# Kernel tuning notes

Hardware: AMD Instinct MI355X
Metric: run time of the kernel (lower is better)

Reference implementation:

```python
import jax, jax.numpy as jnp
import numpy as np

N_NODES = 50000
N_EDGES = 1600000


def setup_inputs() -> dict:
    key = jax.random.key(0)
    ks = jax.random.split(key, 8)
    dims = [1024, 2048, 1024, 512]
    fea = jax.random.normal(ks[0], (N_NODES, dims[0]), dtype=jnp.float32)
    edge_index = jax.random.randint(ks[1], (2, N_EDGES), 0, N_NODES, dtype=jnp.int64)
    edge_vals = jax.random.uniform(ks[2], (N_EDGES,), dtype=jnp.float32)
    # Glorot-ish scaled weights per GCN layer
    W1 = jax.random.normal(ks[3], (dims[0], dims[1]), dtype=jnp.float32) / np.sqrt(dims[0])
    W2 = jax.random.normal(ks[4], (dims[1], dims[2]), dtype=jnp.float32) / np.sqrt(dims[1])
    W3 = jax.random.normal(ks[5], (dims[2], dims[3]), dtype=jnp.float32) / np.sqrt(dims[2])
    b1 = jnp.zeros((dims[1],), dtype=jnp.float32)
    b2 = jnp.zeros((dims[2],), dtype=jnp.float32)
    b3 = jnp.zeros((dims[3],), dtype=jnp.float32)
    return {"fea": fea, "edge_index": edge_index, "edge_vals": edge_vals,
            "W1": W1, "b1": b1, "W2": W2, "b2": b2, "W3": W3, "b3": b3}


def _gcn_layer(x, row, col, edge_vals, W, b):
    # dense transform: [N, din] @ [din, dout] + bias
    support = x @ W + b
    # spmm(adj, support) in COO form: out[row] += val * support[col]
    msgs = support[col] * edge_vals[:, None]          # [E, dout]
    return jax.ops.segment_sum(msgs, row, num_segments=N_NODES)


def reference(fea, edge_index, edge_vals, W1, b1, W2, b2, W3, b3):
    row, col = edge_index[0], edge_index[1]
    h = jax.nn.relu(_gcn_layer(fea, row, col, edge_vals, W1, b1))
    h = jax.nn.relu(_gcn_layer(h, row, col, edge_vals, W2, b2))
    # last layer: no activation
    return _gcn_layer(h, row, col, edge_vals, W3, b3)
```

## Files before the change

### kernel.cpp

```cpp
#include <hip/hip_runtime.h>

typedef unsigned short u16;
using bf16x8 = __attribute__((ext_vector_type(8))) short;
using u16x8  = __attribute__((ext_vector_type(8))) unsigned short;
using f32x4  = __attribute__((ext_vector_type(4))) float;

#define NN 50000
#define NPAD 50176

__device__ __forceinline__ u16 f2b(float f) {
  union { float f; unsigned u; } x; x.f = f;
  unsigned r = x.u + 0x7fffu + ((x.u >> 16) & 1u);
  return (u16)(r >> 16);
}
__device__ __forceinline__ float b2f(u16 h) {
  union { unsigned u; float f; } x; x.u = ((unsigned)h) << 16; return x.f;
}

#define GLOAD_LDS16(g, l) __builtin_amdgcn_global_load_lds( \
    (const __attribute__((address_space(1))) unsigned int*)(g), \
    (__attribute__((address_space(3))) unsigned int*)(l), 16, 0, 0)

__global__ void hist_kernel(const int* __restrict__ rows, const float* __restrict__ vals,
                            int* __restrict__ counts, float* __restrict__ rowsum, int E) {
  int e = blockIdx.x * 256 + threadIdx.x;
  if (e < E) {
    int r = rows[e];
    atomicAdd(&counts[r], 1);
    atomicAdd(&rowsum[r], vals[e]);
  }
}

__global__ void scan_bsum(const int* __restrict__ counts, int* __restrict__ bsum, int n) {
  __shared__ int s[256];
  int t = threadIdx.x;
  int gi = blockIdx.x * 256 + t;
  s[t] = (gi < n) ? counts[gi] : 0;
  __syncthreads();
  for (int d = 128; d > 0; d >>= 1) {
    if (t < d) s[t] += s[t + d];
    __syncthreads();
  }
  if (t == 0) bsum[blockIdx.x] = s[0];
}

__global__ void scan_partials(int* __restrict__ bsum, int nb) {
  __shared__ int s[256];
  int t = threadIdx.x;
  int v = (t < nb) ? bsum[t] : 0;
  s[t] = v;
  __syncthreads();
  for (int d = 1; d < 256; d <<= 1) {
    int x = (t >= d) ? s[t - d] : 0;
    __syncthreads();
    s[t] += x;
    __syncthreads();
  }
  if (t < nb) bsum[t] = s[t] - v;
}

__global__ void scan_final(const int* __restrict__ counts, const int* __restrict__ bsum,
                           int* __restrict__ offs, int n) {
  __shared__ int s[256];
  int t = threadIdx.x;
  int gi = blockIdx.x * 256 + t;
  int v = (gi < n) ? counts[gi] : 0;
  s[t] = v;
  __syncthreads();
  for (int d = 1; d < 256; d <<= 1) {
    int x = (t >= d) ? s[t - d] : 0;
    __syncthreads();
    s[t] += x;
    __syncthreads();
  }
  if (gi <= n) offs[gi] = bsum[blockIdx.x] + s[t] - v;
}

__global__ void scatter_kernel(const int* __restrict__ rows, const int* __restrict__ cols,
                               const float* __restrict__ vals, const int* __restrict__ offs,
                               int* __restrict__ cursor, int* __restrict__ ecol,
                               float* __restrict__ ev2, int E) {
  int e = blockIdx.x * 256 + threadIdx.x;
  if (e < E) {
    int r = rows[e];
    int p = offs[r] + atomicAdd(&cursor[r], 1);
    ecol[p] = cols[e];
    ev2[p] = vals[e];
  }
}

__global__ void conv_f2b4(const float* __restrict__ in, u16* __restrict__ out, int n4) {
  int i = blockIdx.x * 256 + threadIdx.x;
  if (i < n4) {
    float4 f = ((const float4*)in)[i];
    ushort4 o;
    o.x = f2b(f.x); o.y = f2b(f.y); o.z = f2b(f.z); o.w = f2b(f.w);
    ((ushort4*)out)[i] = o;
  }
}

__global__ void transpose_conv(const float* __restrict__ W, u16* __restrict__ Wt, int K, int N) {
  __shared__ float tile[32][33];
  int bx = blockIdx.x * 32;
  int by = blockIdx.y * 32;
  int tx = threadIdx.x;
  int ty = threadIdx.y;
  for (int i = 0; i < 32; i += 8) tile[ty + i][tx] = W[(size_t)(by + ty + i) * N + bx + tx];
  __syncthreads();
  for (int i = 0; i < 32; i += 8) Wt[(size_t)(bx + ty + i) * K + by + tx] = f2b(tile[tx][ty + i]);
}

__global__ __launch_bounds__(512, 2)
void gemm256(const u16* __restrict__ A, const u16* __restrict__ Bt,
             const float* __restrict__ bias, const float* __restrict__ rowsum,
             u16* __restrict__ C, int M, int N, int K, int relu, int nbx) {
  __shared__ __align__(16) u16 As[2][256 * 64];
  __shared__ __align__(16) u16 Bs[2][256 * 64];

  const int p = blockIdx.x, total = gridDim.x;
  const int q = total >> 3, r8 = total & 7;
  const int xcd = p & 7, slot_ = p >> 3;
  const int l = (xcd < r8 ? xcd * (q + 1) : r8 * (q + 1) + (xcd - r8) * q) + slot_;
  const int bm = (l / nbx) * 256;
  const int bn = (l % nbx) * 256;

  const int tid = threadIdx.x;
  const int lane = tid & 63;
  const int wid = tid >> 6;
  const int wm = wid >> 2;
  const int wn = wid & 3;
  const int l15 = lane & 15, lg = lane >> 4;

  const int xcol = (tid & 7) ^ ((tid >> 3) & 7);
  const u16* gA = A + (size_t)(bm + (tid >> 3)) * K + xcol * 8;
  const u16* gB = Bt + (size_t)(bn + (tid >> 3)) * K + xcol * 8;
  const size_t rowstep = (size_t)64 * K;

  f32x4 acc[8][4];
#pragma unroll
  for (int i = 0; i < 8; i++)
#pragma unroll
    for (int j = 0; j < 4; j++)
#pragma unroll
      for (int k = 0; k < 4; k++) acc[i][j][k] = 0.f;

  const int NT = K >> 6;

#define STAGE(kt, b)                                                           \
  {                                                                            \
    const u16* sa = gA + (size_t)(kt) * 64;                                    \
    const u16* sb = gB + (size_t)(kt) * 64;                                    \
    u16* da = &As[b][0] + tid * 8;                                             \
    u16* db = &Bs[b][0] + tid * 8;                                             \
    GLOAD_LDS16(sa, da);                                                       \
    GLOAD_LDS16(sa + rowstep, da + 4096);                                      \
    GLOAD_LDS16(sa + 2 * rowstep, da + 8192);                                  \
    GLOAD_LDS16(sa + 3 * rowstep, da + 12288);                                 \
    GLOAD_LDS16(sb, db);                                                       \
    GLOAD_LDS16(sb + rowstep, db + 4096);                                      \
    GLOAD_LDS16(sb + 2 * rowstep, db + 8192);                                  \
    GLOAD_LDS16(sb + 3 * rowstep, db + 12288);                                 \
  }

  STAGE(0, 0);

  for (int u = 0; u < NT; u++) {
    const int cb = u & 1;
    if (u + 1 < NT) {
      STAGE(u + 1, cb ^ 1);
      asm volatile("s_waitcnt vmcnt(8)" ::: "memory");
    } else {
      asm volatile("s_waitcnt vmcnt(0)" ::: "memory");
    }
    __builtin_amdgcn_s_barrier();

    const u16* ab = &As[cb][0];
    const u16* bb = &Bs[cb][0];

    bf16x8 bf[4][2];
#pragma unroll
    for (int n = 0; n < 4; n++)
#pragma unroll
      for (int s = 0; s < 2; s++) {
        int row = wn * 64 + n * 16 + l15;
        int slot = (s * 4 + lg) ^ (row & 7);
        bf[n][s] = *(const bf16x8*)&bb[row * 64 + slot * 8];
      }
    bf16x8 af0[4][2];
#pragma unroll
    for (int m = 0; m < 4; m++)
#pragma unroll
      for (int s = 0; s < 2; s++) {
        int row = wm * 128 + m * 16 + l15;
        int slot = (s * 4 + lg) ^ (row & 7);
        af0[m][s] = *(const bf16x8*)&ab[row * 64 + slot * 8];
      }
    __builtin_amdgcn_s_setprio(1);
#pragma unroll
    for (int m = 0; m < 4; m++)
#pragma unroll
      for (int n = 0; n < 4; n++) {
        acc[m][n] = __builtin_amdgcn_mfma_f32_16x16x32_bf16(af0[m][0], bf[n][0], acc[m][n], 0, 0, 0);
        acc[m][n] = __builtin_amdgcn_mfma_f32_16x16x32_bf16(af0[m][1], bf[n][1], acc[m][n], 0, 0, 0);
      }
    __builtin_amdgcn_s_setprio(0);
    bf16x8 af1[4][2];
#pragma unroll
    for (int m = 0; m < 4; m++)
#pragma unroll
      for (int s = 0; s < 2; s++) {
        int row = wm * 128 + (m + 4) * 16 + l15;
        int slot = (s * 4 + lg) ^ (row & 7);
        af1[m][s] = *(const bf16x8*)&ab[row * 64 + slot * 8];
      }
    asm volatile("s_waitcnt lgkmcnt(0)" ::: "memory");
    __builtin_amdgcn_s_barrier();
    __builtin_amdgcn_s_setprio(1);
#pragma unroll
    for (int m = 0; m < 4; m++)
#pragma unroll
      for (int n = 0; n < 4; n++) {
        acc[m + 4][n] = __builtin_amdgcn_mfma_f32_16x16x32_bf16(af1[m][0], bf[n][0], acc[m + 4][n], 0, 0, 0);
        acc[m + 4][n] = __builtin_amdgcn_mfma_f32_16x16x32_bf16(af1[m][1], bf[n][1], acc[m + 4][n], 0, 0, 0);
      }
    __builtin_amdgcn_s_setprio(0);
  }
#undef STAGE

  float bs[4];
#pragma unroll
  for (int n = 0; n < 4; n++) bs[n] = bias[bn + wn * 64 + n * 16 + l15];
#pragma unroll
  for (int m = 0; m < 8; m++) {
    int rowb = bm + wm * 128 + m * 16 + lg * 4;
#pragma unroll
    for (int j = 0; j < 4; j++) {
      int row = rowb + j;
      if (row < M) {
        float rs = rowsum ? rowsum[row] : 1.0f;
#pragma unroll
        for (int n = 0; n < 4; n++) {
          int col = bn + wn * 64 + n * 16 + l15;
          float v = acc[m][n][j] + rs * bs[n];
          if (relu) v = fmaxf(v, 0.f);
          C[(size_t)row * N + col] = f2b(v);
        }
      }
    }
  }
}

template <int VEC, int RELU, int OUTF32>
__global__ __launch_bounds__(64)
void spmm3(const int* __restrict__ offs, const int* __restrict__ ecol,
           const float* __restrict__ ev, const u16* __restrict__ X,
           void* __restrict__ outp, int stride) {
  const int node = blockIdx.x;
  const int t = threadIdx.x;
  const int s0 = offs[node];
  const int e0 = offs[node + 1];
  float acc[VEC];
#pragma unroll
  for (int k = 0; k < VEC; k++) acc[k] = 0.f;
  const u16* __restrict__ Xc = X + (size_t)t * VEC;

  int j = s0;
  for (; j + 4 <= e0; j += 4) {
    const int c0 = ecol[j], c1 = ecol[j + 1], c2 = ecol[j + 2], c3 = ecol[j + 3];
    const float v0 = ev[j], v1 = ev[j + 1], v2 = ev[j + 2], v3 = ev[j + 3];
    u16 a0[VEC], a1[VEC], a2[VEC], a3[VEC];
    if constexpr (VEC == 8) {
      *(u16x8*)a0 = *(const u16x8*)(Xc + (size_t)c0 * stride);
      *(u16x8*)a1 = *(const u16x8*)(Xc + (size_t)c1 * stride);
      *(u16x8*)a2 = *(const u16x8*)(Xc + (size_t)c2 * stride);
      *(u16x8*)a3 = *(const u16x8*)(Xc + (size_t)c3 * stride);
    } else {
      *(ushort4*)a0 = *(const ushort4*)(Xc + (size_t)c0 * stride);
      *(ushort4*)a1 = *(const ushort4*)(Xc + (size_t)c1 * stride);
      *(ushort4*)a2 = *(const ushort4*)(Xc + (size_t)c2 * stride);
      *(ushort4*)a3 = *(const ushort4*)(Xc + (size_t)c3 * stride);
    }
#pragma unroll
    for (int k = 0; k < VEC; k++) acc[k] += v0 * b2f(a0[k]);
#pragma unroll
    for (int k = 0; k < VEC; k++) acc[k] += v1 * b2f(a1[k]);
#pragma unroll
    for (int k = 0; k < VEC; k++) acc[k] += v2 * b2f(a2[k]);
#pragma unroll
    for (int k = 0; k < VEC; k++) acc[k] += v3 * b2f(a3[k]);
  }
  for (; j < e0; j++) {
    const int c0 = ecol[j];
    const float v0 = ev[j];
    u16 a0[VEC];
    if constexpr (VEC == 8) {
      *(u16x8*)a0 = *(const u16x8*)(Xc + (size_t)c0 * stride);
    } else {
      *(ushort4*)a0 = *(const ushort4*)(Xc + (size_t)c0 * stride);
    }
#pragma unroll
    for (int k = 0; k < VEC; k++) acc[k] += v0 * b2f(a0[k]);
  }

  if (RELU) {
#pragma unroll
    for (int k = 0; k < VEC; k++) acc[k] = fmaxf(acc[k], 0.f);
  }
  if (OUTF32) {
    float* o = (float*)outp + (size_t)node * stride + (size_t)t * VEC;
#pragma unroll
    for (int k = 0; k < VEC; k += 4) {
      float4 st;
      st.x = acc[k]; st.y = acc[k + 1]; st.z = acc[k + 2]; st.w = acc[k + 3];
      *(float4*)(o + k) = st;
    }
  } else {
    u16* o = (u16*)outp + (size_t)node * stride + (size_t)t * VEC;
    if constexpr (VEC == 8) {
      u16x8 st;
#pragma unroll
      for (int k = 0; k < 8; k++) st[k] = f2b(acc[k]);
      *(u16x8*)o = st;
    } else {
      ushort4 st;
      st.x = f2b(acc[0]); st.y = f2b(acc[1]); st.z = f2b(acc[2]); st.w = f2b(acc[3]);
      *(ushort4*)o = st;
    }
  }
}

extern "C" void kernel_launch(void* const* d_in, const int* in_sizes, int n_in,
                              void* d_out, int out_size, void* d_ws, size_t ws_size,
                              hipStream_t stream) {
  const float* fea = (const float*)d_in[0];
  const int* ei = (const int*)d_in[1];
  const float* ev = (const float*)d_in[2];
  const float* W1 = (const float*)d_in[3];
  const float* b1 = (const float*)d_in[4];
  const float* W2 = (const float*)d_in[5];
  const float* b2 = (const float*)d_in[6];
  const float* W3 = (const float*)d_in[7];
  const float* b3 = (const float*)d_in[8];
  const int E = in_sizes[1] / 2;
  const int* erow = ei;
  const int* ecol_in = ei + E;

  char* w = (char*)d_ws;
  auto alloc = [&](size_t bytes) {
    char* p = w;
    w += (bytes + 255) & ~(size_t)255;
    return p;
  };
  u16* fea_b = (u16*)alloc((size_t)NPAD * 1024 * 2);
  u16* bufB  = (u16*)alloc((size_t)NPAD * 1024 * 2);
  u16* h1_b  = (u16*)alloc((size_t)NPAD * 2048 * 2);
  u16* t2_b  = (u16*)alloc((size_t)NPAD * 1024 * 2);
  u16* W1t = (u16*)alloc((size_t)2048 * 1024 * 2);
  u16* W2t = (u16*)alloc((size_t)1024 * 2048 * 2);
  u16* W3t = (u16*)alloc((size_t)512 * 1024 * 2);
  float* rowsum = (float*)alloc((size_t)NN * 4);
  int* counts = (int*)alloc((size_t)NN * 4);
  int* cursor = (int*)alloc((size_t)NN * 4);
  int* offs = (int*)alloc((size_t)(NN + 1) * 4);
  int* ecol = (int*)alloc((size_t)E * 4);
  float* ev2 = (float*)alloc((size_t)E * 4);
  int* bsum = (int*)alloc(256 * 4);
  (void)bsum; (void)ws_size; (void)n_in; (void)out_size;

  hipMemsetAsync(rowsum, 0, (size_t)((char*)offs - (char*)rowsum), stream);

  const int eb = (E + 255) / 256;
  const int nb = (NN + 256) / 256;
  hist_kernel<<<eb, 256, 0, stream>>>(erow, ev, counts, rowsum, E);
  scan_bsum<<<nb, 256, 0, stream>>>(counts, bsum, NN);
  scan_partials<<<1, 256, 0, stream>>>(bsum, nb);
  scan_final<<<nb, 256, 0, stream>>>(counts, bsum, offs, NN);
  scatter_kernel<<<eb, 256, 0, stream>>>(erow, ecol_in, ev, offs, cursor, ecol, ev2, E);

  conv_f2b4<<<(NN * 1024 / 4 + 255) / 256, 256, 0, stream>>>(fea, fea_b, NN * 1024 / 4);
  dim3 tb(32, 8);
  transpose_conv<<<dim3(2048 / 32, 1024 / 32), tb, 0, stream>>>(W1, W1t, 1024, 2048);
  transpose_conv<<<dim3(1024 / 32, 2048 / 32), tb, 0, stream>>>(W2, W2t, 2048, 1024);
  transpose_conv<<<dim3(512 / 32, 1024 / 32), tb, 0, stream>>>(W3, W3t, 1024, 512);

  const int MT2 = (NN + 255) / 256;
  spmm3<8, 0, 0><<<NN, 64, 0, stream>>>(offs, ecol, ev2, fea_b, bufB, 1024);
  spmm3<8, 0, 0><<<NN, 64, 0, stream>>>(offs, ecol, ev2, fea_b + 512, bufB + 512, 1024);
  gemm256<<<(2048 / 256) * MT2, 512, 0, stream>>>(bufB, W1t, b1, rowsum, h1_b, NN, 2048, 1024, 1, 2048 / 256);
  gemm256<<<(1024 / 256) * MT2, 512, 0, stream>>>(h1_b, W2t, b2, nullptr, t2_b, NN, 1024, 2048, 0, 1024 / 256);
  spmm3<8, 1, 0><<<NN, 64, 0, stream>>>(offs, ecol, ev2, t2_b, fea_b, 1024);
  spmm3<8, 1, 0><<<NN, 64, 0, stream>>>(offs, ecol, ev2, t2_b + 512, fea_b + 512, 1024);
  gemm256<<<(512 / 256) * MT2, 512, 0, stream>>>(fea_b, W3t, b3, nullptr, bufB, NN, 512, 1024, 0, 512 / 256);
  spmm3<4, 0, 1><<<NN, 64, 0, stream>>>(offs, ecol, ev2, bufB, d_out, 512);
  spmm3<4, 0, 1><<<NN, 64, 0, stream>>>(offs, ecol, ev2, bufB + 256, (float*)d_out + 256, 512);
}
```

Measured before the change: 2.103 ms.

## Slice features into 32-column node-contiguous panels for cache-friendly SpMM gathers

The input features and the GEMM outputs that feed SpMM are now stored in a sliced layout: 32-column panels, each holding all nodes contiguously. The SpMM kernel is rewritten so each wave handles one node and one 32-column pass, with four edge groups of 16 lanes reduced by shuffles. Each pass's gather footprint is 64 bytes per node, so the working set per pass fits in L2/MALL and random-row reuse improves. The cost is 64-byte gathers instead of 1 KB row segments per node, extra reduction shuffles, and scattered 2-byte GEMM epilogue stores.

```diff
diff --git a/kernel.cpp b/kernel.cpp
--- a/kernel.cpp
+++ b/kernel.cpp
@@ -89,14 +89,20 @@
   }
 }
 
-__global__ void conv_f2b4(const float* __restrict__ in, u16* __restrict__ out, int n4) {
-  int i = blockIdx.x * 256 + threadIdx.x;
-  if (i < n4) {
-    float4 f = ((const float4*)in)[i];
-    ushort4 o;
-    o.x = f2b(f.x); o.y = f2b(f.y); o.z = f2b(f.z); o.w = f2b(f.w);
-    ((ushort4*)out)[i] = o;
-  }
+__global__ void repack_fea(const float* __restrict__ fea, u16* __restrict__ Xs) {
+  int g = blockIdx.x * 256 + threadIdx.x;
+  if (g >= NN * 128) return;
+  int node = g >> 7;
+  int k = g & 127;
+  const float* src = fea + (size_t)node * 1024 + k * 8;
+  float4 f0 = *(const float4*)src;
+  float4 f1 = *(const float4*)(src + 4);
+  u16x8 o;
+  o[0] = f2b(f0.x); o[1] = f2b(f0.y); o[2] = f2b(f0.z); o[3] = f2b(f0.w);
+  o[4] = f2b(f1.x); o[5] = f2b(f1.y); o[6] = f2b(f1.z); o[7] = f2b(f1.w);
+  int pass = k >> 2;
+  int off = (k & 3) * 8;
+  *(u16x8*)(Xs + (size_t)pass * (NN * 32) + (size_t)node * 32 + off) = o;
 }
 
 __global__ void transpose_conv(const float* __restrict__ W, u16* __restrict__ Wt, int K, int N) {
@@ -113,7 +119,7 @@
 __global__ __launch_bounds__(512, 2)
 void gemm256(const u16* __restrict__ A, const u16* __restrict__ Bt,
              const float* __restrict__ bias, const float* __restrict__ rowsum,
-             u16* __restrict__ C, int M, int N, int K, int relu, int nbx) {
+             u16* __restrict__ C, int M, int N, int K, int relu, int nbx, int sliced) {
   __shared__ __align__(16) u16 As[2][256 * 64];
   __shared__ __align__(16) u16 Bs[2][256 * 64];
 
@@ -243,88 +249,75 @@
           int col = bn + wn * 64 + n * 16 + l15;
           float v = acc[m][n][j] + rs * bs[n];
           if (relu) v = fmaxf(v, 0.f);
-          C[(size_t)row * N + col] = f2b(v);
+          if (!sliced) {
+            C[(size_t)row * N + col] = f2b(v);
+          } else {
+            C[(size_t)(col >> 5) * ((size_t)NN * 32) + (size_t)row * 32 + (col & 31)] = f2b(v);
+          }
         }
       }
     }
   }
 }
 
-template <int VEC, int RELU, int OUTF32>
-__global__ __launch_bounds__(64)
-void spmm3(const int* __restrict__ offs, const int* __restrict__ ecol,
-           const float* __restrict__ ev, const u16* __restrict__ X,
+template <int RELU, int OUTF32>
+__global__ __launch_bounds__(1024)
+void spmm4(const int* __restrict__ offs, const int* __restrict__ ecol,
+           const float* __restrict__ ev, const u16* __restrict__ Xs,
            void* __restrict__ outp, int stride) {
-  const int node = blockIdx.x;
-  const int t = threadIdx.x;
-  const int s0 = offs[node];
-  const int e0 = offs[node + 1];
-  float acc[VEC];
-#pragma unroll
-  for (int k = 0; k < VEC; k++) acc[k] = 0.f;
-  const u16* __restrict__ Xc = X + (size_t)t * VEC;
-
+  const int wid = threadIdx.x >> 6;
+  const int lane = threadIdx.x & 63;
+  const int e2 = lane >> 4;
+  const int c16 = lane & 15;
+  const int bpp = NN / 16;
+  const int pass = blockIdx.x / bpp;
+  const int b = blockIdx.x % bpp;
+  const int q = bpp >> 3, r = bpp & 7;
+  const int xcd = b & 7, slot = b >> 3;
+  const int lb = (xcd < r ? xcd * (q + 1) : r * (q + 1) + (xcd - r) * q) + slot;
+  const int node = lb * 16 + wid;
+
+  const u16* __restrict__ Xp = Xs + (size_t)pass * (NN * 32) + c16 * 2;
+  const int s0 = offs[node], e0 = offs[node + 1];
+  float a0 = 0.f, a1 = 0.f;
   int j = s0;
-  for (; j + 4 <= e0; j += 4) {
-    const int c0 = ecol[j], c1 = ecol[j + 1], c2 = ecol[j + 2], c3 = ecol[j + 3];
-    const float v0 = ev[j], v1 = ev[j + 1], v2 = ev[j + 2], v3 = ev[j + 3];
-    u16 a0[VEC], a1[VEC], a2[VEC], a3[VEC];
-    if constexpr (VEC == 8) {
-      *(u16x8*)a0 = *(const u16x8*)(Xc + (size_t)c0 * stride);
-      *(u16x8*)a1 = *(const u16x8*)(Xc + (size_t)c1 * stride);
-      *(u16x8*)a2 = *(const u16x8*)(Xc + (size_t)c2 * stride);
-      *(u16x8*)a3 = *(const u16x8*)(Xc + (size_t)c3 * stride);
+  for (; j + 8 <= e0; j += 8) {
+    int ca = ecol[j + e2], cb = ecol[j + 4 + e2];
+    float va = ev[j + e2], vb = ev[j + 4 + e2];
+    unsigned pa = *(const unsigned*)(Xp + (size_t)ca * 32);
+    unsigned pb = *(const unsigned*)(Xp + (size_t)cb * 32);
+    a0 += va * b2f((u16)pa);
+    a1 += va * b2f((u16)(pa >> 16));
+    a0 += vb * b2f((u16)pb);
+    a1 += vb * b2f((u16)(pb >> 16));
+  }
+  if (j + 4 <= e0) {
+    int ca = ecol[j + e2];
+    float va = ev[j + e2];
+    unsigned pa = *(const unsigned*)(Xp + (size_t)ca * 32);
+    a0 += va * b2f((u16)pa);
+    a1 += va * b2f((u16)(pa >> 16));
+    j += 4;
+  }
+  if (e2 < e0 - j) {
+    int ca = ecol[j + e2];
+    float va = ev[j + e2];
+    unsigned pa = *(const unsigned*)(Xp + (size_t)ca * 32);
+    a0 += va * b2f((u16)pa);
+    a1 += va * b2f((u16)(pa >> 16));
+  }
+  a0 += __shfl_xor(a0, 16);
+  a1 += __shfl_xor(a1, 16);
+  a0 += __shfl_xor(a0, 32);
+  a1 += __shfl_xor(a1, 32);
+  if (RELU) { a0 = fmaxf(a0, 0.f); a1 = fmaxf(a1, 0.f); }
+  if (e2 == 0) {
+    if (OUTF32) {
+      float2 st; st.x = a0; st.y = a1;
+      *(float2*)((float*)outp + (size_t)node * stride + pass * 32 + c16 * 2) = st;
     } else {
-      *(ushort4*)a0 = *(const ushort4*)(Xc + (size_t)c0 * stride);
-      *(ushort4*)a1 = *(const ushort4*)(Xc + (size_t)c1 * stride);
-      *(ushort4*)a2 = *(const ushort4*)(Xc + (size_t)c2 * stride);
-      *(ushort4*)a3 = *(const ushort4*)(Xc + (size_t)c3 * stride);
-    }
-#pragma unroll
-    for (int k = 0; k < VEC; k++) acc[k] += v0 * b2f(a0[k]);
-#pragma unroll
-    for (int k = 0; k < VEC; k++) acc[k] += v1 * b2f(a1[k]);
-#pragma unroll
-    for (int k = 0; k < VEC; k++) acc[k] += v2 * b2f(a2[k]);
-#pragma unroll
-    for (int k = 0; k < VEC; k++) acc[k] += v3 * b2f(a3[k]);
-  }
-  for (; j < e0; j++) {
-    const int c0 = ecol[j];
-    const float v0 = ev[j];
-    u16 a0[VEC];
-    if constexpr (VEC == 8) {
-      *(u16x8*)a0 = *(const u16x8*)(Xc + (size_t)c0 * stride);
-    } else {
-      *(ushort4*)a0 = *(const ushort4*)(Xc + (size_t)c0 * stride);
-    }
-#pragma unroll
-    for (int k = 0; k < VEC; k++) acc[k] += v0 * b2f(a0[k]);
-  }
-
-  if (RELU) {
-#pragma unroll
-    for (int k = 0; k < VEC; k++) acc[k] = fmaxf(acc[k], 0.f);
-  }
-  if (OUTF32) {
-    float* o = (float*)outp + (size_t)node * stride + (size_t)t * VEC;
-#pragma unroll
-    for (int k = 0; k < VEC; k += 4) {
-      float4 st;
-      st.x = acc[k]; st.y = acc[k + 1]; st.z = acc[k + 2]; st.w = acc[k + 3];
-      *(float4*)(o + k) = st;
-    }
-  } else {
-    u16* o = (u16*)outp + (size_t)node * stride + (size_t)t * VEC;
-    if constexpr (VEC == 8) {
-      u16x8 st;
-#pragma unroll
-      for (int k = 0; k < 8; k++) st[k] = f2b(acc[k]);
-      *(u16x8*)o = st;
-    } else {
-      ushort4 st;
-      st.x = f2b(acc[0]); st.y = f2b(acc[1]); st.z = f2b(acc[2]); st.w = f2b(acc[3]);
-      *(ushort4*)o = st;
+      ushort2 st; st.x = f2b(a0); st.y = f2b(a1);
+      *(ushort2*)((u16*)outp + (size_t)node * stride + pass * 32 + c16 * 2) = st;
     }
   }
 }
@@ -377,20 +370,18 @@
   scan_final<<<nb, 256, 0, stream>>>(counts, bsum, offs, NN);
   scatter_kernel<<<eb, 256, 0, stream>>>(erow, ecol_in, ev, offs, cursor, ecol, ev2, E);
 
-  conv_f2b4<<<(NN * 1024 / 4 + 255) / 256, 256, 0, stream>>>(fea, fea_b, NN * 1024 / 4);
+  repack_fea<<<(NN * 128) / 256, 256, 0, stream>>>(fea, fea_b);
   dim3 tb(32, 8);
   transpose_conv<<<dim3(2048 / 32, 1024 / 32), tb, 0, stream>>>(W1, W1t, 1024, 2048);
   transpose_conv<<<dim3(1024 / 32, 2048 / 32), tb, 0, stream>>>(W2, W2t, 2048, 1024);
   transpose_conv<<<dim3(512 / 32, 1024 / 32), tb, 0, stream>>>(W3, W3t, 1024, 512);
 
   const int MT2 = (NN + 255) / 256;
-  spmm3<8, 0, 0><<<NN, 64, 0, stream>>>(offs, ecol, ev2, fea_b, bufB, 1024);
-  spmm3<8, 0, 0><<<NN, 64, 0, stream>>>(offs, ecol, ev2, fea_b + 512, bufB + 512, 1024);
-  gemm256<<<(2048 / 256) * MT2, 512, 0, stream>>>(bufB, W1t, b1, rowsum, h1_b, NN, 2048, 1024, 1, 2048 / 256);
-  gemm256<<<(1024 / 256) * MT2, 512, 0, stream>>>(h1_b, W2t, b2, nullptr, t2_b, NN, 1024, 2048, 0, 1024 / 256);
-  spmm3<8, 1, 0><<<NN, 64, 0, stream>>>(offs, ecol, ev2, t2_b, fea_b, 1024);
-  spmm3<8, 1, 0><<<NN, 64, 0, stream>>>(offs, ecol, ev2, t2_b + 512, fea_b + 512, 1024);
-  gemm256<<<(512 / 256) * MT2, 512, 0, stream>>>(fea_b, W3t, b3, nullptr, bufB, NN, 512, 1024, 0, 512 / 256);
-  spmm3<4, 0, 1><<<NN, 64, 0, stream>>>(offs, ecol, ev2, bufB, d_out, 512);
-  spmm3<4, 0, 1><<<NN, 64, 0, stream>>>(offs, ecol, ev2, bufB + 256, (float*)d_out + 256, 512);
-}
+  const int BPP = NN / 16;
+  spmm4<0, 0><<<32 * BPP, 1024, 0, stream>>>(offs, ecol, ev2, fea_b, bufB, 1024);
+  gemm256<<<(2048 / 256) * MT2, 512, 0, stream>>>(bufB, W1t, b1, rowsum, h1_b, NN, 2048, 1024, 1, 2048 / 256, 0);
+  gemm256<<<(1024 / 256) * MT2, 512, 0, stream>>>(h1_b, W2t, b2, nullptr, t2_b, NN, 1024, 2048, 0, 1024 / 256, 1);
+  spmm4<1, 0><<<32 * BPP, 1024, 0, stream>>>(offs, ecol, ev2, t2_b, fea_b, 1024);
+  gemm256<<<(512 / 256) * MT2, 512, 0, stream>>>(fea_b, W3t, b3, nullptr, bufB, NN, 512, 1024, 0, 512 / 256, 1);
+  spmm4<0, 1><<<16 * BPP, 1024, 0, stream>>>(offs, ecol, ev2, bufB, d_out, 512);
+}
```

New measurement: 3.148 ms. 1.5x slower.

## Split GEMM main loop into four quadrant phases with interleaved B prefetch

Applied to the files above, without the earlier changes.

Restructures the bf16 MFMA GEMM inner loop into four phases over 2x2 sub-quadrants of the output tile. A and B fragments are loaded in halves, and the next tile's B prefetch is split into two pairs of global-to-LDS loads issued between phases. The goal is to overlap LDS reads and global loads with MFMA work and to cut register pressure from holding all B fragments at once. In exchange it adds more barriers per K-step and a looser vmcnt wait, which could add synchronization stalls.

```diff
diff --git a/kernel.cpp b/kernel.cpp
--- a/kernel.cpp
+++ b/kernel.cpp
@@ -146,86 +146,117 @@
 
   const int NT = K >> 6;
 
-#define STAGE(kt, b)                                                           \
+#define SPAIR_A(kt, b, h)                                                      \
   {                                                                            \
-    const u16* sa = gA + (size_t)(kt) * 64;                                    \
-    const u16* sb = gB + (size_t)(kt) * 64;                                    \
-    u16* da = &As[b][0] + tid * 8;                                             \
-    u16* db = &Bs[b][0] + tid * 8;                                             \
-    GLOAD_LDS16(sa, da);                                                       \
-    GLOAD_LDS16(sa + rowstep, da + 4096);                                      \
-    GLOAD_LDS16(sa + 2 * rowstep, da + 8192);                                  \
-    GLOAD_LDS16(sa + 3 * rowstep, da + 12288);                                 \
-    GLOAD_LDS16(sb, db);                                                       \
-    GLOAD_LDS16(sb + rowstep, db + 4096);                                      \
-    GLOAD_LDS16(sb + 2 * rowstep, db + 8192);                                  \
-    GLOAD_LDS16(sb + 3 * rowstep, db + 12288);                                 \
-  }
-
-  STAGE(0, 0);
+    const u16* s_ = gA + (size_t)(kt) * 64 + (size_t)(2 * (h)) * rowstep;      \
+    u16* d_ = &As[b][0] + tid * 8 + (2 * (h)) * 4096;                          \
+    GLOAD_LDS16(s_, d_);                                                       \
+    GLOAD_LDS16(s_ + rowstep, d_ + 4096);                                      \
+  }
+#define SPAIR_B(kt, b, h)                                                      \
+  {                                                                            \
+    const u16* s_ = gB + (size_t)(kt) * 64 + (size_t)(2 * (h)) * rowstep;      \
+    u16* d_ = &Bs[b][0] + tid * 8 + (2 * (h)) * 4096;                          \
+    GLOAD_LDS16(s_, d_);                                                       \
+    GLOAD_LDS16(s_ + rowstep, d_ + 4096);                                      \
+  }
+
+  SPAIR_A(0, 0, 0); SPAIR_A(0, 0, 1); SPAIR_B(0, 0, 0); SPAIR_B(0, 0, 1);
 
   for (int u = 0; u < NT; u++) {
     const int cb = u & 1;
+    const u16* ab = &As[cb][0];
+    const u16* bb = &Bs[cb][0];
+
     if (u + 1 < NT) {
-      STAGE(u + 1, cb ^ 1);
-      asm volatile("s_waitcnt vmcnt(8)" ::: "memory");
+      SPAIR_A(u + 1, cb ^ 1, 0);
+      SPAIR_A(u + 1, cb ^ 1, 1);
+      asm volatile("s_waitcnt vmcnt(4)" ::: "memory");
     } else {
       asm volatile("s_waitcnt vmcnt(0)" ::: "memory");
     }
     __builtin_amdgcn_s_barrier();
 
-    const u16* ab = &As[cb][0];
-    const u16* bb = &Bs[cb][0];
-
-    bf16x8 bf[4][2];
-#pragma unroll
-    for (int n = 0; n < 4; n++)
-#pragma unroll
-      for (int s = 0; s < 2; s++) {
-        int row = wn * 64 + n * 16 + l15;
-        int slot = (s * 4 + lg) ^ (row & 7);
-        bf[n][s] = *(const bf16x8*)&bb[row * 64 + slot * 8];
-      }
-    bf16x8 af0[4][2];
+    bf16x8 a[4][2], bqa[2][2], bqb[2][2];
+
+#pragma unroll
+    for (int m = 0; m < 4; m++) {
+      int row = wm * 128 + m * 16 + l15, r7 = row & 7;
+#pragma unroll
+      for (int s = 0; s < 2; s++)
+        a[m][s] = *(const bf16x8*)&ab[row * 64 + ((s * 4 + lg) ^ r7) * 8];
+    }
+#pragma unroll
+    for (int n = 0; n < 2; n++) {
+      int row = wn * 64 + n * 16 + l15, r7 = row & 7;
+#pragma unroll
+      for (int s = 0; s < 2; s++)
+        bqa[n][s] = *(const bf16x8*)&bb[row * 64 + ((s * 4 + lg) ^ r7) * 8];
+    }
+    if (u + 1 < NT) SPAIR_B(u + 1, cb ^ 1, 0);
+    __builtin_amdgcn_s_barrier();
+    __builtin_amdgcn_s_setprio(1);
 #pragma unroll
     for (int m = 0; m < 4; m++)
 #pragma unroll
-      for (int s = 0; s < 2; s++) {
-        int row = wm * 128 + m * 16 + l15;
-        int slot = (s * 4 + lg) ^ (row & 7);
-        af0[m][s] = *(const bf16x8*)&ab[row * 64 + slot * 8];
-      }
-    __builtin_amdgcn_s_setprio(1);
-#pragma unroll
-    for (int m = 0; m < 4; m++)
-#pragma unroll
-      for (int n = 0; n < 4; n++) {
-        acc[m][n] = __builtin_amdgcn_mfma_f32_16x16x32_bf16(af0[m][0], bf[n][0], acc[m][n], 0, 0, 0);
-        acc[m][n] = __builtin_amdgcn_mfma_f32_16x16x32_bf16(af0[m][1], bf[n][1], acc[m][n], 0, 0, 0);
+      for (int n = 0; n < 2; n++) {
+        acc[m][n] = __builtin_amdgcn_mfma_f32_16x16x32_bf16(a[m][0], bqa[n][0], acc[m][n], 0, 0, 0);
+        acc[m][n] = __builtin_amdgcn_mfma_f32_16x16x32_bf16(a[m][1], bqa[n][1], acc[m][n], 0, 0, 0);
       }
     __builtin_amdgcn_s_setprio(0);
-    bf16x8 af1[4][2];
+    __builtin_amdgcn_s_barrier();
+
+#pragma unroll
+    for (int n = 0; n < 2; n++) {
+      int row = wn * 64 + (n + 2) * 16 + l15, r7 = row & 7;
+#pragma unroll
+      for (int s = 0; s < 2; s++)
+        bqb[n][s] = *(const bf16x8*)&bb[row * 64 + ((s * 4 + lg) ^ r7) * 8];
+    }
+    if (u + 1 < NT) SPAIR_B(u + 1, cb ^ 1, 1);
+    __builtin_amdgcn_s_barrier();
+    __builtin_amdgcn_s_setprio(1);
 #pragma unroll
     for (int m = 0; m < 4; m++)
 #pragma unroll
-      for (int s = 0; s < 2; s++) {
-        int row = wm * 128 + (m + 4) * 16 + l15;
-        int slot = (s * 4 + lg) ^ (row & 7);
-        af1[m][s] = *(const bf16x8*)&ab[row * 64 + slot * 8];
-      }
-    asm volatile("s_waitcnt lgkmcnt(0)" ::: "memory");
-    __builtin_amdgcn_s_barrier();
-    __builtin_amdgcn_s_setprio(1);
-#pragma unroll
-    for (int m = 0; m < 4; m++)
-#pragma unroll
-      for (int n = 0; n < 4; n++) {
-        acc[m + 4][n] = __builtin_amdgcn_mfma_f32_16x16x32_bf16(af1[m][0], bf[n][0], acc[m + 4][n], 0, 0, 0);
-        acc[m + 4][n] = __builtin_amdgcn_mfma_f32_16x16x32_bf16(af1[m][1], bf[n][1], acc[m + 4][n], 0, 0, 0);
+      for (int n = 0; n < 2; n++) {
+        acc[m][n + 2] = __builtin_amdgcn_mfma_f32_16x16x32_bf16(a[m][0], bqb[n][0], acc[m][n + 2], 0, 0, 0);
+        acc[m][n + 2] = __builtin_amdgcn_mfma_f32_16x16x32_bf16(a[m][1], bqb[n][1], acc[m][n + 2], 0, 0, 0);
       }
     __builtin_amdgcn_s_setprio(0);
-  }
-#undef STAGE
+    __builtin_amdgcn_s_barrier();
+
+#pragma unroll
+    for (int m = 0; m < 4; m++) {
+      int row = wm * 128 + (m + 4) * 16 + l15, r7 = row & 7;
+#pragma unroll
+      for (int s = 0; s < 2; s++)
+        a[m][s] = *(const bf16x8*)&ab[row * 64 + ((s * 4 + lg) ^ r7) * 8];
+    }
+    __builtin_amdgcn_s_barrier();
+    __builtin_amdgcn_s_setprio(1);
+#pragma unroll
+    for (int m = 0; m < 4; m++)
+#pragma unroll
+      for (int n = 0; n < 2; n++) {
+        acc[m + 4][n + 2] = __builtin_amdgcn_mfma_f32_16x16x32_bf16(a[m][0], bqb[n][0], acc[m + 4][n + 2], 0, 0, 0);
+        acc[m + 4][n + 2] = __builtin_amdgcn_mfma_f32_16x16x32_bf16(a[m][1], bqb[n][1], acc[m + 4][n + 2], 0, 0, 0);
+      }
+    __builtin_amdgcn_s_setprio(0);
+    __builtin_amdgcn_s_barrier();
+
+    __builtin_amdgcn_s_setprio(1);
+#pragma unroll
+    for (int m = 0; m < 4; m++)
+#pragma unroll
+      for (int n = 0; n < 2; n++) {
+        acc[m + 4][n] = __builtin_amdgcn_mfma_f32_16x16x32_bf16(a[m][0], bqa[n][0], acc[m + 4][n], 0, 0, 0);
+        acc[m + 4][n] = __builtin_amdgcn_mfma_f32_16x16x32_bf16(a[m][1], bqa[n][1], acc[m + 4][n], 0, 0, 0);
+      }
+    __builtin_amdgcn_s_setprio(0);
+  }
+#undef SPAIR_A
+#undef SPAIR_B
 
   float bs[4];
 #pragma unroll
```

Measured after the change: 2.127 ms. No clear change (+1.2%).

## Shrink GEMM tiles to 256x128x32 for higher occupancy; nontemporal SpMM stores

Applied to the files above, without the earlier changes.

The bf16 MFMA GEMM drops from 256x256 tiles with a K-step of 64 to 256x128 tiles with a K-step of 32. This cuts LDS and accumulator registers so four blocks can be resident per CU, and it rewrites the staging, swizzle, wait counts and launch grids to match. The SpMM output stores become nontemporal. Smaller tiles mean less data reuse per global load and more barriers per unit of K, traded for occupancy and latency hiding.

```diff
diff --git a/kernel.cpp b/kernel.cpp
--- a/kernel.cpp
+++ b/kernel.cpp
@@ -3,6 +3,7 @@
 typedef unsigned short u16;
 using bf16x8 = __attribute__((ext_vector_type(8))) short;
 using u16x8  = __attribute__((ext_vector_type(8))) unsigned short;
+using u16x4  = __attribute__((ext_vector_type(4))) unsigned short;
 using f32x4  = __attribute__((ext_vector_type(4))) float;
 
 #define NN 50000
@@ -110,56 +111,51 @@
   for (int i = 0; i < 32; i += 8) Wt[(size_t)(bx + ty + i) * K + by + tx] = f2b(tile[tx][ty + i]);
 }
 
-__global__ __launch_bounds__(512, 2)
+__global__ __launch_bounds__(512, 4)
 void gemm256(const u16* __restrict__ A, const u16* __restrict__ Bt,
              const float* __restrict__ bias, const float* __restrict__ rowsum,
              u16* __restrict__ C, int M, int N, int K, int relu, int nbx) {
-  __shared__ __align__(16) u16 As[2][256 * 64];
-  __shared__ __align__(16) u16 Bs[2][256 * 64];
+  __shared__ __align__(16) u16 As[2][256 * 32];
+  __shared__ __align__(16) u16 Bs[2][128 * 32];
 
   const int p = blockIdx.x, total = gridDim.x;
   const int q = total >> 3, r8 = total & 7;
   const int xcd = p & 7, slot_ = p >> 3;
   const int l = (xcd < r8 ? xcd * (q + 1) : r8 * (q + 1) + (xcd - r8) * q) + slot_;
   const int bm = (l / nbx) * 256;
-  const int bn = (l % nbx) * 256;
+  const int bn = (l % nbx) * 128;
 
   const int tid = threadIdx.x;
   const int lane = tid & 63;
   const int wid = tid >> 6;
-  const int wm = wid >> 2;
-  const int wn = wid & 3;
+  const int wm = wid >> 1;
+  const int wn = wid & 1;
   const int l15 = lane & 15, lg = lane >> 4;
 
-  const int xcol = (tid & 7) ^ ((tid >> 3) & 7);
-  const u16* gA = A + (size_t)(bm + (tid >> 3)) * K + xcol * 8;
-  const u16* gB = Bt + (size_t)(bn + (tid >> 3)) * K + xcol * 8;
-  const size_t rowstep = (size_t)64 * K;
-
-  f32x4 acc[8][4];
-#pragma unroll
-  for (int i = 0; i < 8; i++)
+  const int trow = tid >> 2;
+  const int xcol = (tid & 3) ^ ((tid >> 3) & 3);
+  const u16* gA = A + (size_t)(bm + trow) * K + xcol * 8;
+  const u16* gB = Bt + (size_t)(bn + trow) * K + xcol * 8;
+  const size_t rowstep = (size_t)128 * K;
+
+  f32x4 acc[4][4];
+#pragma unroll
+  for (int i = 0; i < 4; i++)
 #pragma unroll
     for (int j = 0; j < 4; j++)
 #pragma unroll
       for (int k = 0; k < 4; k++) acc[i][j][k] = 0.f;
 
-  const int NT = K >> 6;
+  const int NT = K >> 5;
 
 #define STAGE(kt, b)                                                           \
   {                                                                            \
-    const u16* sa = gA + (size_t)(kt) * 64;                                    \
-    const u16* sb = gB + (size_t)(kt) * 64;                                    \
+    const u16* sa = gA + (size_t)(kt) * 32;                                    \
     u16* da = &As[b][0] + tid * 8;                                             \
-    u16* db = &Bs[b][0] + tid * 8;                                             \
     GLOAD_LDS16(sa, da);                                                       \
     GLOAD_LDS16(sa + rowstep, da + 4096);                                      \
-    GLOAD_LDS16(sa + 2 * rowstep, da + 8192);                                  \
-    GLOAD_LDS16(sa + 3 * rowstep, da + 12288);                                 \
-    GLOAD_LDS16(sb, db);                                                       \
-    GLOAD_LDS16(sb + rowstep, db + 4096);                                      \
-    GLOAD_LDS16(sb + 2 * rowstep, db + 8192);                                  \
-    GLOAD_LDS16(sb + 3 * rowstep, db + 12288);                                 \
+    const u16* sb = gB + (size_t)(kt) * 32;                                    \
+    GLOAD_LDS16(sb, &Bs[b][0] + tid * 8);                                      \
   }
 
   STAGE(0, 0);
@@ -168,7 +164,7 @@
     const int cb = u & 1;
     if (u + 1 < NT) {
       STAGE(u + 1, cb ^ 1);
-      asm volatile("s_waitcnt vmcnt(8)" ::: "memory");
+      asm volatile("s_waitcnt vmcnt(3)" ::: "memory");
     } else {
       asm volatile("s_waitcnt vmcnt(0)" ::: "memory");
     }
@@ -177,53 +173,26 @@
     const u16* ab = &As[cb][0];
     const u16* bb = &Bs[cb][0];
 
-    bf16x8 bf[4][2];
-#pragma unroll
-    for (int n = 0; n < 4; n++)
-#pragma unroll
-      for (int s = 0; s < 2; s++) {
-        int row = wn * 64 + n * 16 + l15;
-        int slot = (s * 4 + lg) ^ (row & 7);
-        bf[n][s] = *(const bf16x8*)&bb[row * 64 + slot * 8];
-      }
-    bf16x8 af0[4][2];
-#pragma unroll
-    for (int m = 0; m < 4; m++)
-#pragma unroll
-      for (int s = 0; s < 2; s++) {
-        int row = wm * 128 + m * 16 + l15;
-        int slot = (s * 4 + lg) ^ (row & 7);
-        af0[m][s] = *(const bf16x8*)&ab[row * 64 + slot * 8];
-      }
+    bf16x8 bfr[4];
+#pragma unroll
+    for (int n = 0; n < 4; n++) {
+      int row = wn * 64 + n * 16 + l15;
+      int s = lg ^ ((row >> 1) & 3);
+      bfr[n] = *(const bf16x8*)&bb[row * 32 + s * 8];
+    }
     __builtin_amdgcn_s_setprio(1);
 #pragma unroll
-    for (int m = 0; m < 4; m++)
-#pragma unroll
-      for (int n = 0; n < 4; n++) {
-        acc[m][n] = __builtin_amdgcn_mfma_f32_16x16x32_bf16(af0[m][0], bf[n][0], acc[m][n], 0, 0, 0);
-        acc[m][n] = __builtin_amdgcn_mfma_f32_16x16x32_bf16(af0[m][1], bf[n][1], acc[m][n], 0, 0, 0);
-      }
+    for (int m = 0; m < 4; m++) {
+      int row = wm * 64 + m * 16 + l15;
+      int s = lg ^ ((row >> 1) & 3);
+      bf16x8 am = *(const bf16x8*)&ab[row * 32 + s * 8];
+#pragma unroll
+      for (int n = 0; n < 4; n++)
+        acc[m][n] = __builtin_amdgcn_mfma_f32_16x16x32_bf16(am, bfr[n], acc[m][n], 0, 0, 0);
+    }
     __builtin_amdgcn_s_setprio(0);
-    bf16x8 af1[4][2];
-#pragma unroll
-    for (int m = 0; m < 4; m++)
-#pragma unroll
-      for (int s = 0; s < 2; s++) {
-        int row = wm * 128 + (m + 4) * 16 + l15;
-        int slot = (s * 4 + lg) ^ (row & 7);
-        af1[m][s] = *(const bf16x8*)&ab[row * 64 + slot * 8];
-      }
     asm volatile("s_waitcnt lgkmcnt(0)" ::: "memory");
     __builtin_amdgcn_s_barrier();
-    __builtin_amdgcn_s_setprio(1);
-#pragma unroll
-    for (int m = 0; m < 4; m++)
-#pragma unroll
-      for (int n = 0; n < 4; n++) {
-        acc[m + 4][n] = __builtin_amdgcn_mfma_f32_16x16x32_bf16(af1[m][0], bf[n][0], acc[m + 4][n], 0, 0, 0);
-        acc[m + 4][n] = __builtin_amdgcn_mfma_f32_16x16x32_bf16(af1[m][1], bf[n][1], acc[m + 4][n], 0, 0, 0);
-      }
-    __builtin_amdgcn_s_setprio(0);
   }
 #undef STAGE
 
@@ -231,8 +200,8 @@
 #pragma unroll
   for (int n = 0; n < 4; n++) bs[n] = bias[bn + wn * 64 + n * 16 + l15];
 #pragma unroll
-  for (int m = 0; m < 8; m++) {
-    int rowb = bm + wm * 128 + m * 16 + lg * 4;
+  for (int m = 0; m < 4; m++) {
+    int rowb = bm + wm * 64 + m * 16 + lg * 4;
 #pragma unroll
     for (int j = 0; j < 4; j++) {
       int row = rowb + j;
@@ -275,10 +244,10 @@
       *(u16x8*)a2 = *(const u16x8*)(Xc + (size_t)c2 * stride);
       *(u16x8*)a3 = *(const u16x8*)(Xc + (size_t)c3 * stride);
     } else {
-      *(ushort4*)a0 = *(const ushort4*)(Xc + (size_t)c0 * stride);
-      *(ushort4*)a1 = *(const ushort4*)(Xc + (size_t)c1 * stride);
-      *(ushort4*)a2 = *(const ushort4*)(Xc + (size_t)c2 * stride);
-      *(ushort4*)a3 = *(const ushort4*)(Xc + (size_t)c3 * stride);
+      *(u16x4*)a0 = *(const u16x4*)(Xc + (size_t)c0 * stride);
+      *(u16x4*)a1 = *(const u16x4*)(Xc + (size_t)c1 * stride);
+      *(u16x4*)a2 = *(const u16x4*)(Xc + (size_t)c2 * stride);
+      *(u16x4*)a3 = *(const u16x4*)(Xc + (size_t)c3 * stride);
     }
 #pragma unroll
     for (int k = 0; k < VEC; k++) acc[k] += v0 * b2f(a0[k]);
@@ -296,7 +265,7 @@
     if constexpr (VEC == 8) {
       *(u16x8*)a0 = *(const u16x8*)(Xc + (size_t)c0 * stride);
     } else {
-      *(ushort4*)a0 = *(const ushort4*)(Xc + (size_t)c0 * stride);
+      *(u16x4*)a0 = *(const u16x4*)(Xc + (size_t)c0 * stride);
     }
 #pragma unroll
     for (int k = 0; k < VEC; k++) acc[k] += v0 * b2f(a0[k]);
@@ -310,9 +279,9 @@
     float* o = (float*)outp + (size_t)node * stride + (size_t)t * VEC;
 #pragma unroll
     for (int k = 0; k < VEC; k += 4) {
-      float4 st;
-      st.x = acc[k]; st.y = acc[k + 1]; st.z = acc[k + 2]; st.w = acc[k + 3];
-      *(float4*)(o + k) = st;
+      f32x4 st;
+      st[0] = acc[k]; st[1] = acc[k + 1]; st[2] = acc[k + 2]; st[3] = acc[k + 3];
+      __builtin_nontemporal_store(st, (f32x4*)(o + k));
     }
   } else {
     u16* o = (u16*)outp + (size_t)node * stride + (size_t)t * VEC;
@@ -320,11 +289,11 @@
       u16x8 st;
 #pragma unroll
       for (int k = 0; k < 8; k++) st[k] = f2b(acc[k]);
-      *(u16x8*)o = st;
+      __builtin_nontemporal_store(st, (u16x8*)o);
     } else {
-      ushort4 st;
-      st.x = f2b(acc[0]); st.y = f2b(acc[1]); st.z = f2b(acc[2]); st.w = f2b(acc[3]);
-      *(ushort4*)o = st;
+      u16x4 st;
+      st[0] = f2b(acc[0]); st[1] = f2b(acc[1]); st[2] = f2b(acc[2]); st[3] = f2b(acc[3]);
+      __builtin_nontemporal_store(st, (u16x4*)o);
     }
   }
 }
@@ -386,11 +355,11 @@
   const int MT2 = (NN + 255) / 256;
   spmm3<8, 0, 0><<<NN, 64, 0, stream>>>(offs, ecol, ev2, fea_b, bufB, 1024);
   spmm3<8, 0, 0><<<NN, 64, 0, stream>>>(offs, ecol, ev2, fea_b + 512, bufB + 512, 1024);
-  gemm256<<<(2048 / 256) * MT2, 512, 0, stream>>>(bufB, W1t, b1, rowsum, h1_b, NN, 2048, 1024, 1, 2048 / 256);
-  gemm256<<<(1024 / 256) * MT2, 512, 0, stream>>>(h1_b, W2t, b2, nullptr, t2_b, NN, 1024, 2048, 0, 1024 / 256);
+  gemm256<<<(2048 / 128) * MT2, 512, 0, stream>>>(bufB, W1t, b1, rowsum, h1_b, NN, 2048, 1024, 1, 2048 / 128);
+  gemm256<<<(1024 / 128) * MT2, 512, 0, stream>>>(h1_b, W2t, b2, nullptr, t2_b, NN, 1024, 2048, 0, 1024 / 128);
   spmm3<8, 1, 0><<<NN, 64, 0, stream>>>(offs, ecol, ev2, t2_b, fea_b, 1024);
   spmm3<8, 1, 0><<<NN, 64, 0, stream>>>(offs, ecol, ev2, t2_b + 512, fea_b + 512, 1024);
-  gemm256<<<(512 / 256) * MT2, 512, 0, stream>>>(fea_b, W3t, b3, nullptr, bufB, NN, 512, 1024, 0, 512 / 256);
+  gemm256<<<(512 / 128) * MT2, 512, 0, stream>>>(fea_b, W3t, b3, nullptr, bufB, NN, 512, 1024, 0, 512 / 128);
   spmm3<4, 0, 1><<<NN, 64, 0, stream>>>(offs, ecol, ev2, bufB, d_out, 512);
   spmm3<4, 0, 1><<<NN, 64, 0, stream>>>(offs, ecol, ev2, bufB + 256, (float*)d_out + 256, 512);
 }
```

Result: no change. 2.077 ms (-1.2%).
